# Kernel tuning notes

Hardware: AMD Instinct MI355X
Metric: run time of the kernel (lower is better)

Reference implementation:

```python
import jax, jax.numpy as jnp
import numpy as np


def conv1d(x, w, b, pad):
    # x: [B, Cin, T], w: [Cout, Cin, K]
    y = jax.lax.conv_general_dilated(x, w, window_strides=(1,), padding=[(pad, pad)],
                                     dimension_numbers=('NCH', 'OIH', 'NCH'))
    return y + b[None, :, None]


def setup_inputs() -> dict:
    key = jax.random.key(0)
    ks = jax.random.split(key, 16)
    B, T1, T2 = 32, 2048, 512
    Cmel, Ctext, Catt = 100, 512, 100
    s = 0.05
    inp = {
        'queries': jax.random.normal(ks[0], (B, Cmel, T1), dtype=jnp.float32),
        'keys': jax.random.normal(ks[1], (B, Ctext, T2), dtype=jnp.float32),
        'query_lens': jax.random.randint(ks[2], (B,), 1, T1),
        'mask': jax.random.randint(ks[3], (B, T2, 1), 0, 2).astype(bool),
        'attn_prior': jax.random.uniform(ks[4], (B, T1, T2), dtype=jnp.float32),
        # key_proj: ConvNorm(512->1024, k=3) -> ReLU -> ConvNorm(1024->100, k=1)
        'kW1': jax.random.normal(ks[5], (Ctext * 2, Ctext, 3), dtype=jnp.float32) * s,
        'kb1': jnp.zeros((Ctext * 2,), dtype=jnp.float32),
        'kW2': jax.random.normal(ks[6], (Catt, Ctext * 2, 1), dtype=jnp.float32) * s,
        'kb2': jnp.zeros((Catt,), dtype=jnp.float32),
        # query_proj: ConvNorm(100->200, k=3) -> ReLU -> ConvNorm(200->100, k=1) -> ReLU -> ConvNorm(100->100, k=1)
        'qW1': jax.random.normal(ks[7], (Cmel * 2, Cmel, 3), dtype=jnp.float32) * s,
        'qb1': jnp.zeros((Cmel * 2,), dtype=jnp.float32),
        'qW2': jax.random.normal(ks[8], (Cmel, Cmel * 2, 1), dtype=jnp.float32) * s,
        'qb2': jnp.zeros((Cmel,), dtype=jnp.float32),
        'qW3': jax.random.normal(ks[9], (Catt, Cmel, 1), dtype=jnp.float32) * s,
        'qb3': jnp.zeros((Catt,), dtype=jnp.float32),
    }
    return inp


def reference(queries, keys, query_lens, mask, attn_prior,
              kW1, kb1, kW2, kb2, qW1, qb1, qW2, qb2, qW3, qb3):
    # key projection -> [B, Catt, T2]
    k = jax.nn.relu(conv1d(keys, kW1, kb1, 1))
    k = conv1d(k, kW2, kb2, 0)
    # query projection -> [B, Catt, T1]
    q = jax.nn.relu(conv1d(queries, qW1, qb1, 1))
    q = jax.nn.relu(conv1d(q, qW2, qb2, 0))
    q = conv1d(q, qW3, qb3, 0)
    q2 = jnp.sum(q * q, axis=1)                      # [B, T1]
    k2 = jnp.sum(k * k, axis=1)                      # [B, T2]
    qk = jnp.einsum('bct,bcs->bts', q, k)            # [B, T1, T2]
    attn = -0.0005 * (q2[:, :, None] + k2[:, None, :] - 2.0 * qk)[:, None]  # [B,1,T1,T2]
    attn = jax.nn.log_softmax(attn, axis=3) + jnp.log(attn_prior[:, None] + 1e-8)
    attn_logprob = attn
    m = jnp.transpose(mask, (0, 2, 1))[:, :, None, :]  # [B,1,1,T2], True = masked
    attn = jnp.where(m, -jnp.inf, attn)
    attn = jax.nn.softmax(attn, axis=3)
    return attn, attn_logprob
```

## Files before the change

### kernel.cpp

```cpp
#include <hip/hip_runtime.h>
#include <cstdint>

#define B_   32
#define T1_  2048
#define T2_  512

typedef __attribute__((ext_vector_type(8))) short short8;
typedef __attribute__((ext_vector_type(4))) float f32x4;

__device__ __forceinline__ unsigned short f2bf(float f) {
    union { float f; unsigned u; } x; x.f = f;
    unsigned r = x.u + 0x7fffu + ((x.u >> 16) & 1u);
    return (unsigned short)(r >> 16);
}

__device__ __forceinline__ void async16(const unsigned short* g, unsigned short* l) {
    __builtin_amdgcn_global_load_lds(
        (const __attribute__((address_space(1))) unsigned int*)g,
        (__attribute__((address_space(3))) unsigned int*)l, 16, 0, 0);
}

__global__ __launch_bounds__(256) void prep_kernel(
    const float* __restrict__ queries, const float* __restrict__ keys,
    const float* __restrict__ kW1, const float* __restrict__ kW2,
    const float* __restrict__ qW1, const float* __restrict__ qW2,
    const float* __restrict__ qW3,
    unsigned short* __restrict__ keysT, unsigned short* __restrict__ queriesT,
    unsigned short* __restrict__ Wdst)
{
    __shared__ float tile[32][33];
    const int blk = blockIdx.x, tid = threadIdx.x;
    if (blk < 4096) {
        const float* X; unsigned short* Y; int C, Cp, T, ntx, ty, tx0, b;
        if (blk < 2048) {
            X = keys; Y = keysT; C = 512; Cp = 512; T = 512; ntx = 16;
            b = blk >> 6; int rem = blk & 63; ty = rem >> 2; tx0 = (rem & 3) * 4;
        } else {
            int f = blk - 2048;
            X = queries; Y = queriesT; C = 100; Cp = 128; T = 2048; ntx = 64;
            b = f >> 6; int rem = f & 63; ty = rem & 3; tx0 = (rem >> 2) * 4;
        }
        const int c0 = ty * 32;
        const int cl = tid >> 5, tl = tid & 31;
        for (int tx = tx0; tx < tx0 + 4; ++tx) {
            const int t0 = tx * 32;
            __syncthreads();
#pragma unroll
            for (int i = 0; i < 4; ++i) {
                int c = c0 + cl + i * 8;
                float v = (c < C) ? X[((size_t)b * C + c) * T + t0 + tl] : 0.f;
                tile[cl + i * 8][tl] = v;
            }
            __syncthreads();
#pragma unroll
            for (int i = 0; i < 4; ++i) {
                int tw = cl + i * 8, cw = tl;
                Y[((size_t)b * (T + 2) + t0 + tw + 1) * Cp + c0 + cw] = f2bf(tile[cw][tw]);
            }
            if (tid < 32) {
                if (tx == 0)       Y[((size_t)b * (T + 2)) * Cp + c0 + tid] = 0;
                if (tx == ntx - 1) Y[((size_t)b * (T + 2) + T + 1) * Cp + c0 + tid] = 0;
            }
        }
    } else {
        size_t base = (size_t)(blk - 4096) * 2048 + (size_t)tid * 8;
#pragma unroll
        for (int j = 0; j < 8; ++j) {
            size_t idx = base + j;
            float v = 0.f;
            if (idx < 1572864) {
                int dk = (int)(idx / 524288); int rem = (int)(idx % 524288);
                int m = rem >> 9, ci = rem & 511;
                v = kW1[((size_t)m * 512 + ci) * 3 + dk];
            } else if (idx < 1703936) {
                int r = (int)(idx - 1572864); int m = r >> 10, c = r & 1023;
                if (m < 100) v = kW2[(size_t)m * 1024 + c];
            } else if (idx < 1802240) {
                int r = (int)(idx - 1703936); int dk = r / 32768, rem = r % 32768;
                int m = rem >> 7, ci = rem & 127;
                if (m < 200 && ci < 100) v = qW1[((size_t)m * 100 + ci) * 3 + dk];
            } else if (idx < 1835008) {
                int r = (int)(idx - 1802240); int m = r >> 8, c = r & 255;
                if (m < 100 && c < 200) v = qW2[(size_t)m * 200 + c];
            } else if (idx < 1851392) {
                int r = (int)(idx - 1835008); int m = r >> 7, c = r & 127;
                if (m < 100 && c < 100) v = qW3[(size_t)m * 100 + c];
            } else {
                continue;
            }
            Wdst[idx] = f2bf(v);
        }
    }
}

struct GArgs {
    const unsigned short* A;
    const unsigned short* Bm;
    const float* bias;
    unsigned short* Y;
    float* nrm;
    int Ck, N, Mpad, nx, relu, norm, Cout;
    const unsigned short* A2;
    const float* bias2;
    unsigned short* Y2;
    float* nrm2;
    int fuse;
};

template<int KW>
__global__ __launch_bounds__(256) void gemm_pair(GArgs g0, GArgs g1, int n0)
{
    __shared__ __align__(16) unsigned char smem[67584];
    unsigned short* Al = (unsigned short*)smem;
    unsigned short* Ct = (unsigned short*)smem;
    float* biasS  = (float*)(smem + 65536);
    float* bias2S = (float*)(smem + 66048);
    float* normS  = (float*)(smem + 66560);

    const bool first = (blockIdx.x < (unsigned)n0);
    const GArgs g = first ? g0 : g1;
    const int idx = first ? blockIdx.x : (blockIdx.x - n0);
    const int ny = g.Mpad >> 7;
    const int per_b = g.nx * ny;
    const int b = idx / per_b; const int rem = idx - b * per_b;
    const int y = rem / g.nx, x = rem - y * g.nx;
    const int co0 = y * 128, t0 = x * 128;

    const int tid = threadIdx.x;
    const int wave = tid >> 6, lane = tid & 63;
    const int lm = lane & 15, kg = lane >> 4;
    const int mbase = (wave >> 1) * 64, nbase = (wave & 1) * 64;

    if (tid < 128) {
        biasS[tid] = (co0 + tid < g.Cout) ? g.bias[co0 + tid] : 0.f;
        if (g.fuse) bias2S[tid] = (tid < 100) ? g.bias2[tid] : 0.f;
    }

    const int r7 = lane >> 3;
    const int s7 = lane & 7;
    const int swz = ((s7 ^ r7) * 8);
    const int Ck = g.Ck;
    const int ksteps = Ck >> 6;
    const int kshift = __builtin_ctz(ksteps);
    const int nsteps = KW * ksteps;

    auto stage = [&](int s) {
        const int dk = s >> kshift;
        const int kk = (s & (ksteps - 1)) << 6;
        const unsigned short* Ag = g.A + ((size_t)dk * g.Mpad + co0) * Ck + kk;
        const unsigned short* Bg = g.Bm +
            ((size_t)b * (g.N + (KW == 3 ? 2 : 0)) + t0 + dk) * Ck + kk;
        unsigned short* Ad = Al + (s & 1) * 16384;
        unsigned short* Bd = Ad + 8192;
#pragma unroll
        for (int i = 0; i < 4; ++i) {
            int R0 = wave * 32 + i * 8;
            async16(Ag + (size_t)(R0 + r7) * Ck + swz, Ad + R0 * 64);
            async16(Bg + (size_t)(R0 + r7) * Ck + swz, Bd + R0 * 64);
        }
    };

    f32x4 acc[4][4];
#pragma unroll
    for (int mi = 0; mi < 4; ++mi)
#pragma unroll
        for (int ni = 0; ni < 4; ++ni) acc[mi][ni] = (f32x4){0.f, 0.f, 0.f, 0.f};

    stage(0);
    __syncthreads();
#pragma unroll 1
    for (int s = 0; s < nsteps; ++s) {
        if (s + 1 < nsteps) stage(s + 1);
        const unsigned short* Ab = Al + (s & 1) * 16384;
        const unsigned short* Bb = Ab + 8192;
#pragma unroll
        for (int kk2 = 0; kk2 < 2; ++kk2) {
            short8 av[4], bv[4];
#pragma unroll
            for (int mi = 0; mi < 4; ++mi) {
                int row = mbase + mi * 16 + lm;
                av[mi] = *(const short8*)(Ab + row * 64 +
                                          (((kk2 * 4 + kg) ^ (lm & 7)) * 8));
            }
#pragma unroll
            for (int ni = 0; ni < 4; ++ni) {
                int row = nbase + ni * 16 + lm;
                bv[ni] = *(const short8*)(Bb + row * 64 +
                                          (((kk2 * 4 + kg) ^ (lm & 7)) * 8));
            }
#pragma unroll
            for (int mi = 0; mi < 4; ++mi)
#pragma unroll
                for (int ni = 0; ni < 4; ++ni)
                    acc[mi][ni] = __builtin_amdgcn_mfma_f32_16x16x32_bf16(
                        av[mi], bv[ni], acc[mi][ni], 0, 0, 0);
        }
        __syncthreads();
    }

    auto epi = [&](f32x4 (&A)[4][4], const float* bS, int dorelu, int donorm) {
        float sq[4] = {0.f, 0.f, 0.f, 0.f};
#pragma unroll
        for (int mi = 0; mi < 4; ++mi)
#pragma unroll
            for (int ni = 0; ni < 4; ++ni)
#pragma unroll
                for (int r = 0; r < 4; ++r) {
                    int co_l = mbase + mi * 16 + kg * 4 + r;
                    int t_l  = nbase + ni * 16 + lm;
                    float v = A[mi][ni][r] + bS[co_l];
                    if (dorelu) v = fmaxf(v, 0.f);
                    Ct[t_l * 136 + co_l] = f2bf(v);
                    sq[ni] += v * v;
                }
        if (donorm) {
#pragma unroll
            for (int ni = 0; ni < 4; ++ni) {
                float s = sq[ni];
                s += __shfl_xor(s, 16, 64);
                s += __shfl_xor(s, 32, 64);
                if (kg == 0) normS[(wave >> 1) * 128 + nbase + ni * 16 + lm] = s;
            }
        }
    };

    if (!g.fuse) {
        epi(acc, biasS, g.relu, g.norm);
        __syncthreads();
        unsigned short* Yb = g.Y + ((size_t)b * g.N + t0) * g.Mpad + co0;
        int c0 = (tid & 15) * 8;
#pragma unroll
        for (int p = 0; p < 8; ++p) {
            int r = (tid >> 4) + p * 16;
            *(uint4*)(Yb + (size_t)r * g.Mpad + c0) = *(const uint4*)(Ct + r * 136 + c0);
        }
        if (g.norm && tid < 128)
            g.nrm[(size_t)b * g.N + t0 + tid] = normS[tid] + normS[128 + tid];
    } else {
        epi(acc, biasS, 1, 0);
        __syncthreads();
        f32x4 acc2[4][4];
#pragma unroll
        for (int mi = 0; mi < 4; ++mi)
#pragma unroll
            for (int ni = 0; ni < 4; ++ni) acc2[mi][ni] = (f32x4){0.f, 0.f, 0.f, 0.f};
#pragma unroll
        for (int kk = 0; kk < 128; kk += 32) {
            short8 av2[4], bv2[4];
#pragma unroll
            for (int mi = 0; mi < 4; ++mi)
                av2[mi] = *(const short8*)(g.A2 +
                    (size_t)(mbase + mi * 16 + lm) * 128 + kk + kg * 8);
#pragma unroll
            for (int ni = 0; ni < 4; ++ni)
                bv2[ni] = *(const short8*)(Ct +
                    (nbase + ni * 16 + lm) * 136 + kk + kg * 8);
#pragma unroll
            for (int mi = 0; mi < 4; ++mi)
#pragma unroll
                for (int ni = 0; ni < 4; ++ni)
                    acc2[mi][ni] = __builtin_amdgcn_mfma_f32_16x16x32_bf16(
                        av2[mi], bv2[ni], acc2[mi][ni], 0, 0, 0);
        }
        __syncthreads();
        epi(acc2, bias2S, 0, 1);
        __syncthreads();
        unsigned short* Yb = g.Y2 + ((size_t)b * g.N + t0) * 128 + co0;
        int c0 = (tid & 15) * 8;
#pragma unroll
        for (int p = 0; p < 8; ++p) {
            int r = (tid >> 4) + p * 16;
            *(uint4*)(Yb + (size_t)r * 128 + c0) = *(const uint4*)(Ct + r * 136 + c0);
        }
        if (tid < 128)
            g.nrm2[(size_t)b * g.N + t0 + tid] = normS[tid] + normS[128 + tid];
    }
}

__global__ __launch_bounds__(256) void attn_mfma(
    const unsigned short* __restrict__ q,
    const unsigned short* __restrict__ k,
    const float* __restrict__ q2,
    const float* __restrict__ k2,
    const unsigned char* __restrict__ mask,
    const float* __restrict__ prior,
    float* __restrict__ out_attn, float* __restrict__ out_logp)
{
    __shared__ float redM[4][32], redS[4][32];
    __shared__ float rowA[32], rowB[32];

    const int b = blockIdx.y, t0 = blockIdx.x * 32;
    const int tid = threadIdx.x, wave = tid >> 6, lane = tid & 63;
    const int lm = lane & 15, quad = lane >> 4;
    const float NEG_INF = -__builtin_huge_valf();

    const unsigned short* qb = q + ((size_t)b * T1_ + t0) * 128;
    short8 af[2][4];
#pragma unroll
    for (int mi = 0; mi < 2; ++mi)
#pragma unroll
        for (int kb = 0; kb < 4; ++kb)
            af[mi][kb] = *(const short8*)(qb + (size_t)(mi * 16 + lm) * 128 + kb * 32 + quad * 8);

    f32x4 acc[2][8];
#pragma unroll
    for (int mi = 0; mi < 2; ++mi)
#pragma unroll
        for (int nf = 0; nf < 8; ++nf) acc[mi][nf] = (f32x4){0.f, 0.f, 0.f, 0.f};

    const unsigned short* kp = k + ((size_t)b * T2_ + wave * 128) * 128;
#pragma unroll
    for (int nf = 0; nf < 8; ++nf) {
        short8 bfr[4];
#pragma unroll
        for (int kb = 0; kb < 4; ++kb)
            bfr[kb] = *(const short8*)(kp + (size_t)(nf * 16 + lm) * 128 + kb * 32 + quad * 8);
#pragma unroll
        for (int mi = 0; mi < 2; ++mi)
#pragma unroll
            for (int kb = 0; kb < 4; ++kb)
                acc[mi][nf] = __builtin_amdgcn_mfma_f32_16x16x32_bf16(
                    af[mi][kb], bfr[kb], acc[mi][nf], 0, 0, 0);
    }

    float k2v[8];
    unsigned char mk[8];
#pragma unroll
    for (int nf = 0; nf < 8; ++nf) {
        int col = wave * 128 + nf * 16 + lm;
        k2v[nf] = k2[b * T2_ + col];
        mk[nf]  = mask[b * T2_ + col];
    }
    float q2v[2][4];
#pragma unroll
    for (int mi = 0; mi < 2; ++mi)
#pragma unroll
        for (int r = 0; r < 4; ++r)
            q2v[mi][r] = q2[b * T1_ + t0 + mi * 16 + quad * 4 + r];
#pragma unroll
    for (int mi = 0; mi < 2; ++mi)
#pragma unroll
        for (int nf = 0; nf < 8; ++nf)
#pragma unroll
            for (int r = 0; r < 4; ++r)
                acc[mi][nf][r] = 1e-3f * acc[mi][nf][r] - 5e-4f * (q2v[mi][r] + k2v[nf]);

#pragma unroll
    for (int mi = 0; mi < 2; ++mi)
#pragma unroll
        for (int r = 0; r < 4; ++r) {
            float m = NEG_INF;
#pragma unroll
            for (int nf = 0; nf < 8; ++nf) m = fmaxf(m, acc[mi][nf][r]);
#pragma unroll
            for (int d = 1; d <= 8; d <<= 1) m = fmaxf(m, __shfl_xor(m, d, 64));
            float s = 0.f;
#pragma unroll
            for (int nf = 0; nf < 8; ++nf) s += __expf(acc[mi][nf][r] - m);
#pragma unroll
            for (int d = 1; d <= 8; d <<= 1) s += __shfl_xor(s, d, 64);
            if (lm == 0) {
                redM[wave][mi * 16 + quad * 4 + r] = m;
                redS[wave][mi * 16 + quad * 4 + r] = s;
            }
        }
    __syncthreads();
    if (tid < 32) {
        float m = redM[0][tid];
        m = fmaxf(m, redM[1][tid]); m = fmaxf(m, redM[2][tid]); m = fmaxf(m, redM[3][tid]);
        float s = 0.f;
#pragma unroll
        for (int w = 0; w < 4; ++w) s += redS[w][tid] * __expf(redM[w][tid] - m);
        rowA[tid] = m + __logf(s);
    }
    __syncthreads();
    float L1[2][4];
#pragma unroll
    for (int mi = 0; mi < 2; ++mi)
#pragma unroll
        for (int r = 0; r < 4; ++r) L1[mi][r] = rowA[mi * 16 + quad * 4 + r];

    const size_t base = ((size_t)b * T1_ + t0) * T2_;
#pragma unroll
    for (int mi = 0; mi < 2; ++mi)
#pragma unroll
        for (int r = 0; r < 4; ++r) {
            size_t rowoff = base + (size_t)(mi * 16 + quad * 4 + r) * T2_;
#pragma unroll
            for (int nf = 0; nf < 8; ++nf) {
                int col = wave * 128 + nf * 16 + lm;
                float pv = prior[rowoff + col];
                float t = acc[mi][nf][r] + __logf(pv + 1e-8f);
                out_logp[rowoff + col] = t - L1[mi][r];
                acc[mi][nf][r] = mk[nf] ? NEG_INF : t;
            }
        }

#pragma unroll
    for (int mi = 0; mi < 2; ++mi)
#pragma unroll
        for (int r = 0; r < 4; ++r) {
            float m = NEG_INF;
#pragma unroll
            for (int nf = 0; nf < 8; ++nf) m = fmaxf(m, acc[mi][nf][r]);
#pragma unroll
            for (int d = 1; d <= 8; d <<= 1) m = fmaxf(m, __shfl_xor(m, d, 64));
            float s = 0.f;
#pragma unroll
            for (int nf = 0; nf < 8; ++nf) s += __expf(acc[mi][nf][r] - m);
#pragma unroll
            for (int d = 1; d <= 8; d <<= 1) s += __shfl_xor(s, d, 64);
            if (lm == 0) {
                redM[wave][mi * 16 + quad * 4 + r] = m;
                redS[wave][mi * 16 + quad * 4 + r] = s;
            }
        }
    __syncthreads();
    if (tid < 32) {
        float m = redM[0][tid];
        m = fmaxf(m, redM[1][tid]); m = fmaxf(m, redM[2][tid]); m = fmaxf(m, redM[3][tid]);
        float s = 0.f;
#pragma unroll
        for (int w = 0; w < 4; ++w) s += redS[w][tid] * __expf(redM[w][tid] - m);
        rowA[tid] = m;
        rowB[tid] = 1.0f / s;
    }
    __syncthreads();

#pragma unroll
    for (int mi = 0; mi < 2; ++mi)
#pragma unroll
        for (int r = 0; r < 4; ++r) {
            int rl = mi * 16 + quad * 4 + r;
            float m2 = rowA[rl], is2 = rowB[rl];
            size_t rowoff = base + (size_t)rl * T2_;
#pragma unroll
            for (int nf = 0; nf < 8; ++nf) {
                int col = wave * 128 + nf * 16 + lm;
                out_attn[rowoff + col] = __expf(acc[mi][nf][r] - m2) * is2;
            }
        }
}

extern "C" void kernel_launch(void* const* d_in, const int* in_sizes, int n_in,
                              void* d_out, int out_size, void* d_ws, size_t ws_size,
                              hipStream_t stream)
{
    const float* queries = (const float*)d_in[0];
    const float* keys    = (const float*)d_in[1];
    const unsigned char* mask = (const unsigned char*)d_in[3];
    const float* prior   = (const float*)d_in[4];
    const float* kW1 = (const float*)d_in[5];
    const float* kb1 = (const float*)d_in[6];
    const float* kW2 = (const float*)d_in[7];
    const float* kb2 = (const float*)d_in[8];
    const float* qW1 = (const float*)d_in[9];
    const float* qb1 = (const float*)d_in[10];
    const float* qW2 = (const float*)d_in[11];
    const float* qb2 = (const float*)d_in[12];
    const float* qW3 = (const float*)d_in[13];
    const float* qb3 = (const float*)d_in[14];

    unsigned short* ws = (unsigned short*)d_ws;
    unsigned short* keysT    = ws;
    unsigned short* queriesT = ws + 8421376;
    unsigned short* Bmat2    = ws + 16818176;
    unsigned short* Bmat4    = ws + 33595392;
    unsigned short* q_att    = ws + 58761216;
    unsigned short* k_att    = ws + 67149824;
    unsigned short* Wdst     = ws + 69246976;
    unsigned short* Wk1s = Wdst;
    unsigned short* Wk2  = Wdst + 1572864;
    unsigned short* Wq1s = Wdst + 1703936;
    unsigned short* Wq2  = Wdst + 1802240;
    unsigned short* Wq3  = Wdst + 1835008;
    float* q2f = (float*)(ws + 71098368);
    float* k2f = q2f + 65536;

    float* out_attn = (float*)d_out;
    float* out_logp = (float*)d_out + (size_t)B_ * T1_ * T2_;

    dim3 blk(256);
    prep_kernel<<<dim3(5120), blk, 0, stream>>>(queries, keys, kW1, kW2, qW1, qW2, qW3,
                                                keysT, queriesT, Wdst);

    GArgs a_key1 = {Wk1s, keysT,    kb1, Bmat2, nullptr, 512,  512, 1024,  4, 1, 0, 1024,
                    nullptr, nullptr, nullptr, nullptr, 0};
    GArgs a_q1   = {Wq1s, queriesT, qb1, Bmat4, nullptr, 128, 2048,  256, 16, 1, 0,  200,
                    nullptr, nullptr, nullptr, nullptr, 0};
    gemm_pair<3><<<dim3(2048), blk, 0, stream>>>(a_key1, a_q1, 1024);

    GArgs a_key2 = {Wk2, Bmat2, kb2, k_att, k2f,     1024,  512, 128,  4, 0, 1, 100,
                    nullptr, nullptr, nullptr, nullptr, 0};
    GArgs a_q23  = {Wq2, Bmat4, qb2, nullptr, nullptr, 256, 2048, 128, 16, 1, 0, 100,
                    Wq3, qb3, q_att, q2f, 1};
    gemm_pair<1><<<dim3(640), blk, 0, stream>>>(a_key2, a_q23, 128);

    attn_mfma<<<dim3(T1_ / 32, B_), blk, 0, stream>>>(q_att, k_att, q2f, k2f, mask, prior,
                                                      out_attn, out_logp);

    (void)in_sizes; (void)n_in; (void)out_size; (void)ws_size;
}
```

Baseline: 591.3 us.

## Deepen conv GEMM pipeline to four stages with 32-wide K steps

Result: slower. 604.3 us (+2.2%).

```diff
diff --git a/kernel.cpp b/kernel.cpp
--- a/kernel.cpp
+++ b/kernel.cpp
@@ -136,27 +136,26 @@
         if (g.fuse) bias2S[tid] = (tid < 100) ? g.bias2[tid] : 0.f;
     }
 
-    const int r7 = lane >> 3;
-    const int s7 = lane & 7;
-    const int swz = ((s7 ^ r7) * 8);
+    const int r16 = lane >> 2;
+    const int sl  = (lane & 3) * 8;
     const int Ck = g.Ck;
-    const int ksteps = Ck >> 6;
+    const int ksteps = Ck >> 5;
     const int kshift = __builtin_ctz(ksteps);
     const int nsteps = KW * ksteps;
 
     auto stage = [&](int s) {
         const int dk = s >> kshift;
-        const int kk = (s & (ksteps - 1)) << 6;
+        const int kk = (s & (ksteps - 1)) << 5;
         const unsigned short* Ag = g.A + ((size_t)dk * g.Mpad + co0) * Ck + kk;
         const unsigned short* Bg = g.Bm +
             ((size_t)b * (g.N + (KW == 3 ? 2 : 0)) + t0 + dk) * Ck + kk;
-        unsigned short* Ad = Al + (s & 1) * 16384;
-        unsigned short* Bd = Ad + 8192;
-#pragma unroll
-        for (int i = 0; i < 4; ++i) {
-            int R0 = wave * 32 + i * 8;
-            async16(Ag + (size_t)(R0 + r7) * Ck + swz, Ad + R0 * 64);
-            async16(Bg + (size_t)(R0 + r7) * Ck + swz, Bd + R0 * 64);
+        unsigned short* Ad = Al + (s & 3) * 8192;
+        unsigned short* Bd = Ad + 4096;
+#pragma unroll
+        for (int i = 0; i < 2; ++i) {
+            int R0 = wave * 32 + i * 16;
+            async16(Ag + (size_t)(R0 + r16) * Ck + sl, Ad + R0 * 32);
+            async16(Bg + (size_t)(R0 + r16) * Ck + sl, Bd + R0 * 32);
         }
     };
 
@@ -166,36 +165,43 @@
 #pragma unroll
         for (int ni = 0; ni < 4; ++ni) acc[mi][ni] = (f32x4){0.f, 0.f, 0.f, 0.f};
 
-    stage(0);
-    __syncthreads();
+    if (nsteps > 0) stage(0);
+    if (nsteps > 1) stage(1);
+    if (nsteps > 2) stage(2);
+
 #pragma unroll 1
     for (int s = 0; s < nsteps; ++s) {
-        if (s + 1 < nsteps) stage(s + 1);
-        const unsigned short* Ab = Al + (s & 1) * 16384;
-        const unsigned short* Bb = Ab + 8192;
-#pragma unroll
-        for (int kk2 = 0; kk2 < 2; ++kk2) {
-            short8 av[4], bv[4];
-#pragma unroll
-            for (int mi = 0; mi < 4; ++mi) {
-                int row = mbase + mi * 16 + lm;
-                av[mi] = *(const short8*)(Ab + row * 64 +
-                                          (((kk2 * 4 + kg) ^ (lm & 7)) * 8));
-            }
-#pragma unroll
-            for (int ni = 0; ni < 4; ++ni) {
-                int row = nbase + ni * 16 + lm;
-                bv[ni] = *(const short8*)(Bb + row * 64 +
-                                          (((kk2 * 4 + kg) ^ (lm & 7)) * 8));
-            }
-#pragma unroll
-            for (int mi = 0; mi < 4; ++mi)
-#pragma unroll
-                for (int ni = 0; ni < 4; ++ni)
-                    acc[mi][ni] = __builtin_amdgcn_mfma_f32_16x16x32_bf16(
-                        av[mi], bv[ni], acc[mi][ni], 0, 0, 0);
-        }
-        __syncthreads();
+        const int remn = nsteps - s;
+        if (remn > 3) {
+            stage(s + 3);
+            asm volatile("s_waitcnt vmcnt(12)" ::: "memory");
+        } else if (remn == 3) {
+            asm volatile("s_waitcnt vmcnt(8)" ::: "memory");
+        } else if (remn == 2) {
+            asm volatile("s_waitcnt vmcnt(4)" ::: "memory");
+        } else {
+            asm volatile("s_waitcnt vmcnt(0)" ::: "memory");
+        }
+        __builtin_amdgcn_s_barrier();
+
+        const unsigned short* Ab = Al + (s & 3) * 8192;
+        const unsigned short* Bb = Ab + 4096;
+        short8 av[4], bv[4];
+#pragma unroll
+        for (int mi = 0; mi < 4; ++mi)
+            av[mi] = *(const short8*)(Ab + (mbase + mi * 16 + lm) * 32 + kg * 8);
+#pragma unroll
+        for (int ni = 0; ni < 4; ++ni)
+            bv[ni] = *(const short8*)(Bb + (nbase + ni * 16 + lm) * 32 + kg * 8);
+#pragma unroll
+        for (int mi = 0; mi < 4; ++mi)
+#pragma unroll
+            for (int ni = 0; ni < 4; ++ni)
+                acc[mi][ni] = __builtin_amdgcn_mfma_f32_16x16x32_bf16(
+                    av[mi], bv[ni], acc[mi][ni], 0, 0, 0);
+
+        asm volatile("s_waitcnt lgkmcnt(0)" ::: "memory");
+        __builtin_amdgcn_s_barrier();
     }
 
     auto epi = [&](f32x4 (&A)[4][4], const float* bS, int dorelu, int donorm) {
```
